# Optimization experiments

Measured on AMD Instinct MI355X. Metric: run time of the kernel, lower is better.

Reference implementation:

```python
import jax, jax.numpy as jnp
import numpy as np

B, T, N, PRED, DM = 16, 512, 128, 256, 32
L = T + PRED  # 768; conv windows 12 then 4: 768 -> 64 -> 16
EPS = 1e-5


def _conv1d(x, w, b, stride):
    # x: [B, C, L'], w: [C, C, k], kernel_size == stride, VALID (matches torch Conv1d)
    out = jax.lax.conv_general_dilated(x, w, (stride,), 'VALID',
                                       dimension_numbers=('NCH', 'OIH', 'NCH'))
    return out + b[None, :, None]


def _conv2d(x, w, b, pad):
    out = jax.lax.conv_general_dilated(x, w, (1, 1), [(pad, pad), (pad, pad)],
                                       dimension_numbers=('NCHW', 'OIHW', 'NCHW'))
    return out + b[None, :, None, None]


def _bn1d(x, g, b):
    # BatchNorm1d, training-mode batch statistics over (batch, length) per channel
    mu = x.mean((0, 2), keepdims=True)
    var = ((x - mu) ** 2).mean((0, 2), keepdims=True)
    return (x - mu) * jax.lax.rsqrt(var + EPS) * g[None, :, None] + b[None, :, None]


def _cubic_spline(y, size):
    # Natural cubic spline through values y: [B, Lk, C] at knots t = linspace(0,1,Lk),
    # evaluated at linspace(0,1,size). Natural BC: second derivative M=0 at endpoints.
    Bb, Lk, C = y.shape
    h = 1.0 / (Lk - 1)
    # tridiagonal system for interior second derivatives (uniform knots):
    # M[i-1] + 4 M[i] + M[i+1] = 6 * (y[i+1] - 2 y[i] + y[i-1]) / h^2
    m = Lk - 2
    rhs = (y[:, 2:, :] - 2.0 * y[:, 1:-1, :] + y[:, :-2, :]) * (6.0 / (h * h))  # [B,m,C]
    A = 4.0 * jnp.eye(m, dtype=y.dtype) + jnp.eye(m, k=1, dtype=y.dtype) + jnp.eye(m, k=-1, dtype=y.dtype)
    Mi = jnp.linalg.solve(A, rhs.transpose(1, 0, 2).reshape(m, Bb * C))  # [m, B*C]
    Mi = Mi.reshape(m, Bb, C).transpose(1, 0, 2)
    M = jnp.pad(Mi, ((0, 0), (1, 1), (0, 0)))  # [B, Lk, C], M[0]=M[-1]=0
    q = jnp.linspace(0.0, 1.0, size).astype(y.dtype)
    idx = jnp.clip(jnp.floor(q * (Lk - 1)).astype(jnp.int32), 0, Lk - 2)  # [size]
    s = (q - idx.astype(y.dtype) * h)[None, :, None]  # offset within interval
    u = h - s
    yi, yi1 = y[:, idx, :], y[:, idx + 1, :]
    M0, M1 = M[:, idx, :], M[:, idx + 1, :]
    hh6 = h * h / 6.0
    return ((M0 * u ** 3 + M1 * s ** 3) / (6.0 * h)
            + (yi - M0 * hh6) * (u / h)
            + (yi1 - M1 * hh6) * (s / h))  # [B, size, C]


def _forward(batch_x, le_w, le_b, c1_w, c1_b, bn1_g, bn1_b, c2_w, c2_b, bn2_g, bn2_b,
             i1_w0, i1_b0, i1_w1, i1_b1, i2_w0, i2_b0, i2_w1, i2_b1, ld_w, ld_b):
    # instance norm over time
    means = batch_x.mean(1, keepdims=True)
    xc = batch_x - means
    stdev = jnp.sqrt(xc.var(axis=1, keepdims=True) + EPS)
    xn = xc / stdev                               # [B, T, N]
    x = xn.transpose(0, 2, 1)                     # [B, N, T]
    x = jnp.einsum('bnt,lt->bnl', x, le_w) + le_b  # length_encoder -> [B, N, L]
    # multi-scale downsampling conv + spline back up to L
    scales = []
    t = x
    for win, cw, cb, g, bb in ((12, c1_w, c1_b, bn1_g, bn1_b), (4, c2_w, c2_b, bn2_g, bn2_b)):
        t = jax.nn.elu(_bn1d(_conv1d(t, cw, cb, win), g, bb))      # [B, N, L//...]
        scales.append(_cubic_spline(t.transpose(0, 2, 1), L).transpose(0, 2, 1))  # [B, N, L]
    a = jnp.stack([x] + scales, axis=1).transpose(0, 1, 3, 2)  # [B, 3, L, N]
    # Inception block 1 (num_kernels=2: 1x1 and 3x3, averaged), Dropout(eval)=id, GELU(exact)
    h1 = 0.5 * (_conv2d(a, i1_w0, i1_b0, 0) + _conv2d(a, i1_w1, i1_b1, 1))  # [B, DM, L, N]
    h1 = jax.nn.gelu(h1, approximate=False)
    # Inception block 2 -> 1 channel
    h2 = 0.5 * (_conv2d(h1, i2_w0, i2_b0, 0) + _conv2d(h1, i2_w1, i2_b1, 1))  # [B, 1, L, N]
    co = x + h2[:, 0].transpose(0, 2, 1)          # residual, [B, N, L]
    f = jnp.einsum('bnl,pl->bnp', co, ld_w) + ld_b  # length_decoder -> [B, N, PRED]
    f = f.transpose(0, 2, 1)                      # [B, PRED, N]
    return f * stdev[:, 0, :][:, None, :] + means[:, 0, :][:, None, :]


def setup_inputs():
    key = jax.random.key(0)
    ks = jax.random.split(key, 20)
    def w(i, shape, scale=0.02):
        return scale * jax.random.normal(ks[i], shape, jnp.float32)
    return dict(
        batch_x=jax.random.normal(ks[0], (B, T, N), jnp.float32),
        batch_x_mark=jax.random.normal(ks[1], (B, T, 4), jnp.float32),
        dec_inp=jax.random.normal(ks[2], (B, PRED, N), jnp.float32),
        batch_y_mark=jax.random.normal(ks[3], (B, PRED, 4), jnp.float32),
        le_w=w(4, (L, T)), le_b=w(5, (L,)),
        c1_w=w(6, (N, N, 12)), c1_b=w(7, (N,)),
        bn1_g=jnp.ones((N,), jnp.float32), bn1_b=jnp.zeros((N,), jnp.float32),
        c2_w=w(8, (N, N, 4)), c2_b=w(9, (N,)),
        bn2_g=jnp.ones((N,), jnp.float32), bn2_b=jnp.zeros((N,), jnp.float32),
        i1_w0=w(10, (DM, 3, 1, 1), 0.1), i1_b0=jnp.zeros((DM,), jnp.float32),
        i1_w1=w(11, (DM, 3, 3, 3), 0.1), i1_b1=jnp.zeros((DM,), jnp.float32),
        i2_w0=w(12, (1, DM, 1, 1), 0.1), i2_b0=jnp.zeros((1,), jnp.float32),
        i2_w1=w(13, (1, DM, 3, 3), 0.1), i2_b1=jnp.zeros((1,), jnp.float32),
        ld_w=w(14, (PRED, L)), ld_b=w(15, (PRED,)),
    )


def reference(batch_x, batch_x_mark, dec_inp, batch_y_mark, le_w, le_b,
              c1_w, c1_b, bn1_g, bn1_b, c2_w, c2_b, bn2_g, bn2_b,
              i1_w0, i1_b0, i1_w1, i1_b1, i2_w0, i2_b0, i2_w1, i2_b1, ld_w, ld_b):
    # batch_x_mark / dec_inp / batch_y_mark are accepted but unused (as in the torch forward)
    return _forward(batch_x, le_w, le_b, c1_w, c1_b, bn1_g, bn1_b, c2_w, c2_b, bn2_g, bn2_b,
                    i1_w0, i1_b0, i1_w1, i1_b1, i2_w0, i2_b0, i2_w1, i2_b1, ld_w, ld_b)
```

## Files before the change

kernel.cpp:

```cpp
#include <hip/hip_runtime.h>
#include <hip/hip_bf16.h>
#include <math.h>

#define BB 16
#define TT 512
#define NN 128
#define PREDN 256
#define DMC 32
#define LL 768
constexpr float EPSF = 1e-5f;
using bf16 = __hip_bfloat16;
using frag_ab = __attribute__((ext_vector_type(8))) short;
using frag_cd = __attribute__((ext_vector_type(4))) float;

__device__ __forceinline__ unsigned pbf2(float a, float b){
  union { bf16 h; unsigned short u; } x, y;
  x.h = __float2bfloat16(a); y.h = __float2bfloat16(b);
  return (unsigned)x.u | ((unsigned)y.u << 16);
}

__device__ __forceinline__ unsigned short bf16b(float v){
  union { bf16 h; unsigned short u; } x;
  x.h = __float2bfloat16(v);
  return x.u;
}

__device__ __forceinline__ float gelu_fast(float s){
  float s2v = s*s;
  float e = exp2f(s*fmaf(s2v, 0.10294396f, 2.30211806f));
  return s*e*__builtin_amdgcn_rcpf(e + 1.f);
}

__global__ void k_pre(const float* __restrict__ bx, const float* __restrict__ v0,
                      const float* __restrict__ v1, const float* __restrict__ w1c,
                      const float* __restrict__ w2c, float* __restrict__ sp,
                      float* __restrict__ s2p, float* __restrict__ vwsT,
                      float* __restrict__ wT1, float* __restrict__ wT2){
  int blk = blockIdx.x;
  if(blk < 64){
    int b = blk >> 2, tq = blk & 3, n = threadIdx.x;
    const float* p = bx + (size_t)b*TT*NN + (size_t)tq*128*NN + n;
    float s = 0.f, s2 = 0.f;
    for(int t=0;t<128;t++){ float v = p[(size_t)t*NN]; s += v; s2 += v*v; }
    sp[tq*2048 + b*NN + n] = s;
    s2p[tq*2048 + b*NN + n] = s2;
  } else if(blk == 64){
    for(int i=threadIdx.x; i<9*DMC; i+=blockDim.x){
      int tap = i/DMC, c = i%DMC;
      float wv = 0.5f*v1[c*9 + tap];
      if(tap == 4) wv += 0.5f*v0[c];
      vwsT[i] = wv;
    }
  } else if(blk <= 192){
    int o = blk - 65;
    for(int k=threadIdx.x; k<1536; k+=blockDim.x)
      wT1[(size_t)k*NN + o] = w1c[(size_t)o*1536 + k];
  } else {
    int o = blk - 193;
    for(int k=threadIdx.x; k<512; k+=blockDim.x)
      wT2[(size_t)k*NN + o] = w2c[(size_t)o*512 + k];
  }
}

__global__ __launch_bounds__(256) void k_gemm1(const float* __restrict__ bx, const float* __restrict__ lew,
    const float* __restrict__ leb, const float* __restrict__ sp, const float* __restrict__ s2p,
    float* __restrict__ x, float* __restrict__ a0){
  __shared__ unsigned Asu[64*20];
  __shared__ unsigned Bsu[64*20];
  int tid = threadIdx.x;
  int row0 = blockIdx.x*64, l0 = blockIdx.y*64;
  int b = row0 >> 7, n0 = row0 & 127;
  int lane = tid & 63, wv = tid >> 6;
  frag_cd acc[4] = {};
  int an = tid & 63, akq = (tid >> 6)*8;
  float mu_a, rs_a;
  {
    int rowa = row0 + an;
    float ssum = 0.f, s2sum = 0.f;
    #pragma unroll
    for(int tq=0;tq<4;tq++){ ssum += sp[tq*2048 + rowa]; s2sum += s2p[tq*2048 + rowa]; }
    mu_a = ssum*(1.f/512.f);
    rs_a = 1.f/sqrtf(fmaxf(s2sum*(1.f/512.f) - mu_a*mu_a, 0.f) + EPSF);
  }
  int btk = tid & 15, blc = tid >> 4;
  unsigned ra[4], rbq[4];
  #pragma unroll
  for(int u=0;u<4;u++){
    float v0 = (bx[((size_t)b*TT + akq + 2*u)*NN + n0 + an] - mu_a)*rs_a;
    float v1 = (bx[((size_t)b*TT + akq + 2*u + 1)*NN + n0 + an] - mu_a)*rs_a;
    ra[u] = pbf2(v0, v1);
    const float* lp = lew + (size_t)(l0 + blc + 16*u)*TT + 2*btk;
    rbq[u] = pbf2(lp[0], lp[1]);
  }
  int fr = wv*16 + (lane & 15);
  int fq = (lane >> 4)*4;
  for(int k0=0;k0<TT;k0+=32){
    *(uint4*)&Asu[an*20 + (akq>>1)] = make_uint4(ra[0], ra[1], ra[2], ra[3]);
    #pragma unroll
    for(int p=0;p<4;p++) Bsu[(blc + 16*p)*20 + btk] = rbq[p];
    __syncthreads();
    if(k0 + 32 < TT){
      #pragma unroll
      for(int u=0;u<4;u++){
        float v0 = (bx[((size_t)b*TT + k0 + 32 + akq + 2*u)*NN + n0 + an] - mu_a)*rs_a;
        float v1 = (bx[((size_t)b*TT + k0 + 32 + akq + 2*u + 1)*NN + n0 + an] - mu_a)*rs_a;
        ra[u] = pbf2(v0, v1);
        const float* lp = lew + (size_t)(l0 + blc + 16*u)*TT + k0 + 32 + 2*btk;
        rbq[u] = pbf2(lp[0], lp[1]);
      }
    }
    frag_ab af = *(const frag_ab*)&Asu[fr*20 + fq];
    #pragma unroll
    for(int nt=0;nt<4;nt++){
      frag_ab bf = *(const frag_ab*)&Bsu[(nt*16 + (lane & 15))*20 + fq];
      acc[nt] = __builtin_amdgcn_mfma_f32_16x16x32_bf16(af, bf, acc[nt], 0, 0, 0);
    }
    __syncthreads();
  }
  int col = lane & 15, quad = lane >> 4;
  #pragma unroll
  for(int nt=0;nt<4;nt++){
    int l = l0 + nt*16 + col;
    float lb = leb[l];
    #pragma unroll
    for(int r=0;r<4;r++){
      int m = wv*16 + quad*4 + r;
      x[(size_t)(row0 + m)*LL + l] = acc[nt][r] + lb;
    }
    float4 st;
    st.x = acc[nt][0] + lb;
    st.y = acc[nt][1] + lb;
    st.z = acc[nt][2] + lb;
    st.w = acc[nt][3] + lb;
    *(float4*)&a0[((size_t)b*LL + l)*NN + n0 + wv*16 + quad*4] = st;
  }
}

__global__ __launch_bounds__(512) void k_conv1(const float* __restrict__ x, const float* __restrict__ wT,
                                               const float* __restrict__ bias, float* __restrict__ t1){
  __shared__ alignas(16) float xs[NN*48];
  int jt = blockIdx.x, b = blockIdx.y;
  int tid = threadIdx.x;
  int o = tid & 127, jj = tid >> 7;
  for(int i=tid;i<NN*48;i+=512){
    int ci = i/48, kk = i%48;
    xs[i] = x[((size_t)b*NN + ci)*LL + jt*48 + kk];
  }
  __syncthreads();
  float a0 = 0.f, a1 = 0.f, a2 = 0.f, a3 = 0.f;
  for(int ci=0;ci<NN;ci++){
    const float* xc = xs + ci*48 + jj*12;
    const float* wc = wT + (size_t)(ci*12)*NN + o;
    #pragma unroll
    for(int kk=0;kk<12;kk+=4){
      a0 = fmaf(xc[kk+0], wc[(size_t)(kk+0)*NN], a0);
      a1 = fmaf(xc[kk+1], wc[(size_t)(kk+1)*NN], a1);
      a2 = fmaf(xc[kk+2], wc[(size_t)(kk+2)*NN], a2);
      a3 = fmaf(xc[kk+3], wc[(size_t)(kk+3)*NN], a3);
    }
  }
  int j = jt*4 + jj;
  t1[((size_t)b*NN + o)*64 + j] = (a0 + a1) + (a2 + a3) + bias[o];
}

__global__ void k_bnstats(const float* __restrict__ t, const float* __restrict__ g, const float* __restrict__ bb,
                          int Bcnt, int Jcnt, float* __restrict__ scale, float* __restrict__ shift){
  int o = blockIdx.x;
  int tot = Bcnt*Jcnt;
  float s = 0.f, s2 = 0.f;
  for(int i=threadIdx.x; i<tot; i+=blockDim.x){
    int b = i / Jcnt, j = i % Jcnt;
    float v = t[((size_t)b*NN + o)*Jcnt + j];
    s += v; s2 += v*v;
  }
  __shared__ float rs[256], rs2[256];
  rs[threadIdx.x] = s; rs2[threadIdx.x] = s2;
  __syncthreads();
  for(int st=128; st>0; st>>=1){
    if(threadIdx.x < st){ rs[threadIdx.x] += rs[threadIdx.x+st]; rs2[threadIdx.x] += rs2[threadIdx.x+st]; }
    __syncthreads();
  }
  if(threadIdx.x == 0){
    float mu = rs[0]/tot;
    float var = fmaxf(rs2[0]/tot - mu*mu, 0.f);
    float sc = g[o] * rsqrtf(var + EPSF);
    scale[o] = sc; shift[o] = bb[o] - mu*sc;
  }
}

__global__ void k_bnelu_t(const float* __restrict__ t, const float* __restrict__ scale,
                          const float* __restrict__ shift, int Jcnt, float* __restrict__ tt){
  int j = blockIdx.x, b = blockIdx.y, o = threadIdx.x;
  float v = t[((size_t)b*NN + o)*Jcnt + j]*scale[o] + shift[o];
  v = v > 0.f ? v : (expf(v) - 1.f);
  tt[((size_t)b*Jcnt + j)*NN + o] = v;
}

template<int LK>
__global__ void k_spline_solve(const float* __restrict__ y, float* __restrict__ M){
  constexpr int m = LK-2;
  const float Kc = 6.f*(LK-1)*(LK-1);
  __shared__ float cp[m];
  __shared__ float dp[m][NN];
  int b = blockIdx.x, c = threadIdx.x;
  if(c == 0){
    float cv = 0.25f; cp[0] = cv;
    for(int i=1;i<m;i++){ cv = 1.f/(4.f - cv); cp[i] = cv; }
  }
  __syncthreads();
  const float* yb = y + (size_t)b*LK*NN + c;
  float y0 = yb[0], y1 = yb[NN];
  float dprev = 0.f;
  for(int i=0;i<m;i++){
    float y2 = yb[(size_t)(i+2)*NN];
    float r = (y2 - 2.f*y1 + y0)*Kc;
    float d = (i == 0) ? r*0.25f : (r - dprev)*cp[i];
    dp[i][c] = d; dprev = d;
    y0 = y1; y1 = y2;
  }
  float* Mb = M + (size_t)b*LK*NN + c;
  float xv = dp[m-1][c];
  Mb[(size_t)m*NN] = xv;
  for(int i=m-2;i>=0;i--){
    xv = dp[i][c] - cp[i]*xv;
    Mb[(size_t)(i+1)*NN] = xv;
  }
  Mb[0] = 0.f;
  Mb[(size_t)(LK-1)*NN] = 0.f;
}

__device__ __forceinline__ float spline_pt(const float* __restrict__ y, const float* __restrict__ M,
                                           int LK, int l, int b, int c){
  float hh = 1.f/(LK-1);
  float q = (float)l * (1.f/(LL-1));
  int idx = (int)floorf(q*(LK-1));
  if(idx > LK-2) idx = LK-2;
  float s = q - idx*hh;
  float u = hh - s;
  const float* yb = y + ((size_t)b*LK + idx)*NN + c;
  const float* Mb = M + ((size_t)b*LK + idx)*NN + c;
  float yi = yb[0], yi1 = yb[NN], M0 = Mb[0], M1 = Mb[NN];
  float hh6 = hh*hh/6.f;
  return (M0*u*u*u + M1*s*s*s)*(1.f/(6.f*hh))
       + (yi  - M0*hh6)*(u*(1.f/hh))
       + (yi1 - M1*hh6)*(s*(1.f/hh));
}

__global__ __launch_bounds__(512) void k_conv2(const float* __restrict__ tt, const float* __restrict__ wT,
                                               const float* __restrict__ bias, float* __restrict__ t2){
  __shared__ alignas(16) float ts[16*NN];
  int jt = blockIdx.x, b = blockIdx.y;
  int tid = threadIdx.x;
  int o = tid & 127, jj = tid >> 7;
  for(int i=tid;i<16*NN;i+=512)
    ts[i] = tt[((size_t)b*64 + jt*16)*NN + i];
  __syncthreads();
  float a0 = 0.f, a1 = 0.f, a2 = 0.f, a3 = 0.f;
  for(int ci=0;ci<NN;ci++){
    const float* wc = wT + (size_t)(ci*4)*NN + o;
    const float* tc2 = ts + (jj*4)*NN + ci;
    a0 = fmaf(tc2[0*NN], wc[0*NN], a0);
    a1 = fmaf(tc2[1*NN], wc[1*NN], a1);
    a2 = fmaf(tc2[2*NN], wc[2*NN], a2);
    a3 = fmaf(tc2[3*NN], wc[3*NN], a3);
  }
  int j = jt*4 + jj;
  t2[((size_t)b*NN + o)*16 + j] = (a0 + a1) + (a2 + a3) + bias[o];
}

constexpr int KOFF[27] = {
    0,   1,   2,  36,  37,  38,  72,  73,  74,
  432, 433, 434, 468, 469, 470, 504, 505, 506,
  864, 865, 866, 900, 901, 902, 936, 937, 938
};

__global__ __launch_bounds__(256) void k_h12(const float* __restrict__ a0,
    const float* __restrict__ y64, const float* __restrict__ M64,
    const float* __restrict__ y16, const float* __restrict__ M16,
    const float* __restrict__ w0, const float* __restrict__ b0,
    const float* __restrict__ w1, const float* __restrict__ b1,
    const float* __restrict__ vwsT, const float* __restrict__ vb0,
    const float* __restrict__ vb1, float* __restrict__ co){
  constexpr int AR = 12, AC = 36;
  __shared__ alignas(16) float as[3][AR][AC];
  __shared__ alignas(16) unsigned Au[352*20];
  int tid = threadIdx.x;
  int l0 = blockIdx.x*8, n0 = blockIdx.y*32, b = blockIdx.z;
  int lane = tid & 63, wv = tid >> 6;

  float* asf = &as[0][0][0];
  for(int i=tid; i<3*AR*AC; i+=256){
    int ch = i/(AR*AC), rem = i%(AR*AC), yy = rem/AC, xx = rem%AC;
    int gl = l0 + yy - 2, gn = n0 + xx - 2;
    float v = 0.f;
    if(gl >= 0 && gl < LL && gn >= 0 && gn < NN){
      if(ch == 0)      v = a0[((size_t)b*LL + gl)*NN + gn];
      else if(ch == 1) v = spline_pt(y64, M64, 64, gl, b, gn);
      else             v = spline_pt(y16, M16, 16, gl, b, gn);
    }
    asf[i] = v;
  }

  int colB = lane & 15, kq = (lane >> 4)*8;
  union { uint4 q; frag_ab f; } bw0, bw1;
  {
    float w8[2][8];
    #pragma unroll
    for(int nt=0;nt<2;nt++){
      #pragma unroll
      for(int j=0;j<8;j++){
        int k = kq + j;
        float w = 0.f;
        if(k < 27){
          int ci = k/9, r9 = k - ci*9, dy = r9/3, dx = r9 - dy*3;
          int c = nt*16 + colB;
          w = 0.5f*w1[((c*3+ci)*3+dy)*3+dx];
          if(dy==1 && dx==1) w += 0.5f*w0[c*3+ci];
        }
        w8[nt][j] = w;
      }
    }
    bw0.q = make_uint4(pbf2(w8[0][0],w8[0][1]), pbf2(w8[0][2],w8[0][3]),
                       pbf2(w8[0][4],w8[0][5]), pbf2(w8[0][6],w8[0][7]));
    bw1.q = make_uint4(pbf2(w8[1][0],w8[1][1]), pbf2(w8[1][2],w8[1][3]),
                       pbf2(w8[1][4],w8[1][5]), pbf2(w8[1][6],w8[1][7]));
  }
  float br0 = 0.5f*(b0[colB] + b1[colB]);
  float br1 = 0.5f*(b0[16 + colB] + b1[16 + colB]);
  __syncthreads();

  for(int base=0; base<352; base+=128){
    int px = base + (tid >> 1);
    int half = tid & 1;
    if(px < 352){
      uint4 oA, oB;
      if(px < 340){
        int yy = px/34, xx = px - yy*34;
        const float* bp = asf + yy*AC + xx;
        if(half == 0){
          oA.x = pbf2(bp[KOFF[0]],  bp[KOFF[1]]);
          oA.y = pbf2(bp[KOFF[2]],  bp[KOFF[3]]);
          oA.z = pbf2(bp[KOFF[4]],  bp[KOFF[5]]);
          oA.w = pbf2(bp[KOFF[6]],  bp[KOFF[7]]);
          oB.x = pbf2(bp[KOFF[8]],  bp[KOFF[9]]);
          oB.y = pbf2(bp[KOFF[10]], bp[KOFF[11]]);
          oB.z = pbf2(bp[KOFF[12]], bp[KOFF[13]]);
          oB.w = pbf2(bp[KOFF[14]], bp[KOFF[15]]);
        } else {
          oA.x = pbf2(bp[KOFF[16]], bp[KOFF[17]]);
          oA.y = pbf2(bp[KOFF[18]], bp[KOFF[19]]);
          oA.z = pbf2(bp[KOFF[20]], bp[KOFF[21]]);
          oA.w = pbf2(bp[KOFF[22]], bp[KOFF[23]]);
          oB.x = pbf2(bp[KOFF[24]], bp[KOFF[25]]);
          oB.y = pbf2(bp[KOFF[26]], 0.f);
          oB.z = 0u; oB.w = 0u;
        }
      } else {
        oA = make_uint4(0u,0u,0u,0u);
        oB = make_uint4(0u,0u,0u,0u);
      }
      *(uint4*)&Au[px*20 + half*8]     = oA;
      *(uint4*)&Au[px*20 + half*8 + 4] = oB;
    }
  }
  __syncthreads();

  unsigned short* h1h = (unsigned short*)Au;
  frag_cd zac = {0.f, 0.f, 0.f, 0.f};
  for(int t = wv; t < 22; t += 4){
    int arow = t*16 + colB;
    union { uint4 q; frag_ab f; } av;
    av.q = *(const uint4*)&Au[arow*20 + (lane>>4)*4];
    frag_cd d0 = __builtin_amdgcn_mfma_f32_16x16x32_bf16(av.f, bw0.f, zac, 0, 0, 0);
    frag_cd d1 = __builtin_amdgcn_mfma_f32_16x16x32_bf16(av.f, bw1.f, zac, 0, 0, 0);
    int px0 = t*16 + (lane>>4)*4;
    #pragma unroll
    for(int r=0;r<4;r++){
      int px = px0 + r;
      h1h[px*40 + colB]      = bf16b(gelu_fast(d0[r] + br0));
      h1h[px*40 + 16 + colB] = bf16b(gelu_fast(d1[r] + br1));
    }
  }
  __syncthreads();

  if(n0 == 0){
    for(int i=tid;i<10*32;i+=256){ int yy=i>>5, ch=i&31; h1h[(yy*34)*40 + ch] = 0; }
  }
  if(n0 == 96){
    for(int i=tid;i<10*32;i+=256){ int yy=i>>5, ch=i&31; h1h[(yy*34+33)*40 + ch] = 0; }
  }
  if(l0 == 0){
    for(int i=tid;i<34*32;i+=256){ int xx=i>>5, ch=i&31; h1h[xx*40 + ch] = 0; }
  }
  if(l0 == 760){
    for(int i=tid;i<34*32;i+=256){ int xx=i>>5, ch=i&31; h1h[(9*34+xx)*40 + ch] = 0; }
  }

  union { uint4 q; frag_ab f; } aw[9];
  {
    bool wlane = (lane & 15) == 0;
    int c8 = (lane >> 4)*8;
    #pragma unroll
    for(int tap=0; tap<9; tap++){
      const float* wp = vwsT + tap*DMC + c8;
      float4 wa = *(const float4*)wp;
      float4 wb = *(const float4*)(wp+4);
      if(!wlane){ wa = make_float4(0.f,0.f,0.f,0.f); wb = make_float4(0.f,0.f,0.f,0.f); }
      aw[tap].q = make_uint4(pbf2(wa.x,wa.y), pbf2(wa.z,wa.w), pbf2(wb.x,wb.y), pbf2(wb.z,wb.w));
    }
  }
  float vbsum = vb0[0] + vb1[0];
  __syncthreads();

  frag_cd cacc[4] = {};
  int kq4 = (lane >> 4)*4;
  int baseoff[4];
  #pragma unroll
  for(int tt=0; tt<4; tt++){
    int px = (wv*4 + tt)*16 + (lane & 15);
    int yy = px >> 5, xx = px & 31;
    baseoff[tt] = (yy*34 + xx)*20 + kq4;
  }
  #pragma unroll
  for(int dy=0; dy<3; dy++)
    #pragma unroll
    for(int dx=0; dx<3; dx++){
      int tap = dy*3 + dx;
      int off = (dy*34 + dx)*20;
      #pragma unroll
      for(int tt=0; tt<4; tt++){
        union { uint4 q; frag_ab f; } bv;
        bv.q = *(const uint4*)&Au[baseoff[tt] + off];
        cacc[tt] = __builtin_amdgcn_mfma_f32_16x16x32_bf16(aw[tap].f, bv.f, cacc[tt], 0, 0, 0);
      }
    }
  if(lane < 16){
    #pragma unroll
    for(int tt=0; tt<4; tt++){
      int px = (wv*4 + tt)*16 + lane;
      int yy = px >> 5, xx = px & 31;
      float res = as[0][yy+2][xx+2];
      size_t idx = ((size_t)b*LL + l0 + yy)*NN + n0 + xx;
      co[idx] = cacc[tt][0] + vbsum + res;
    }
  }
}

__global__ __launch_bounds__(256) void k_gemm2(const float* __restrict__ a0, const float* __restrict__ ldw,
    const float* __restrict__ ldb, const float* __restrict__ sp, const float* __restrict__ s2p,
    float* __restrict__ out){
  __shared__ unsigned Asu[64*20];
  __shared__ unsigned Bsu[64*20];
  int tid = threadIdx.x;
  int row0 = blockIdx.x*64, p0 = blockIdx.y*64;
  int b = row0 >> 7, n0 = row0 & 127;
  int lane = tid & 63, wv = tid >> 6;
  frag_cd acc[4] = {};
  int an = tid & 63, akq = (tid >> 6)*8;
  int btk = tid & 15, blc = tid >> 4;
  unsigned ra[4], rbq[4];
  #pragma unroll
  for(int u=0;u<4;u++){
    float v0 = a0[((size_t)b*LL + akq + 2*u)*NN + n0 + an];
    float v1 = a0[((size_t)b*LL + akq + 2*u + 1)*NN + n0 + an];
    ra[u] = pbf2(v0, v1);
    const float* lp = ldw + (size_t)(p0 + blc + 16*u)*LL + 2*btk;
    rbq[u] = pbf2(lp[0], lp[1]);
  }
  int fr = wv*16 + (lane & 15);
  int fq = (lane >> 4)*4;
  for(int k0=0;k0<LL;k0+=32){
    *(uint4*)&Asu[an*20 + (akq>>1)] = make_uint4(ra[0], ra[1], ra[2], ra[3]);
    #pragma unroll
    for(int p=0;p<4;p++) Bsu[(blc + 16*p)*20 + btk] = rbq[p];
    __syncthreads();
    if(k0 + 32 < LL){
      #pragma unroll
      for(int u=0;u<4;u++){
        float v0 = a0[((size_t)b*LL + k0 + 32 + akq + 2*u)*NN + n0 + an];
        float v1 = a0[((size_t)b*LL + k0 + 32 + akq + 2*u + 1)*NN + n0 + an];
        ra[u] = pbf2(v0, v1);
        const float* lp = ldw + (size_t)(p0 + blc + 16*u)*LL + k0 + 32 + 2*btk;
        rbq[u] = pbf2(lp[0], lp[1]);
      }
    }
    frag_ab af = *(const frag_ab*)&Asu[fr*20 + fq];
    #pragma unroll
    for(int nt=0;nt<4;nt++){
      frag_ab bf = *(const frag_ab*)&Bsu[(nt*16 + (lane & 15))*20 + fq];
      acc[nt] = __builtin_amdgcn_mfma_f32_16x16x32_bf16(af, bf, acc[nt], 0, 0, 0);
    }
    __syncthreads();
  }
  int col = lane & 15, quad = lane >> 4;
  float mu_r[4], sd_r[4];
  #pragma unroll
  for(int r=0;r<4;r++){
    int row = row0 + wv*16 + quad*4 + r;
    float ssum = 0.f, s2sum = 0.f;
    #pragma unroll
    for(int tq=0;tq<4;tq++){ ssum += sp[tq*2048 + row]; s2sum += s2p[tq*2048 + row]; }
    float mu = ssum*(1.f/512.f);
    float var = fmaxf(s2sum*(1.f/512.f) - mu*mu, 0.f);
    mu_r[r] = mu; sd_r[r] = sqrtf(var + EPSF);
  }
  #pragma unroll
  for(int nt=0;nt<4;nt++){
    int p = p0 + nt*16 + col;
    float lb = ldb[p];
    float4 st;
    st.x = (acc[nt][0] + lb)*sd_r[0] + mu_r[0];
    st.y = (acc[nt][1] + lb)*sd_r[1] + mu_r[1];
    st.z = (acc[nt][2] + lb)*sd_r[2] + mu_r[2];
    st.w = (acc[nt][3] + lb)*sd_r[3] + mu_r[3];
    *(float4*)&out[((size_t)b*PREDN + p)*NN + n0 + wv*16 + quad*4] = st;
  }
}

extern "C" void kernel_launch(void* const* d_in, const int* in_sizes, int n_in,
                              void* d_out, int out_size, void* d_ws, size_t ws_size,
                              hipStream_t stream){
  (void)in_sizes; (void)n_in; (void)out_size; (void)ws_size;
  const float* batch_x = (const float*)d_in[0];
  const float* le_w  = (const float*)d_in[4];
  const float* le_b  = (const float*)d_in[5];
  const float* c1_w  = (const float*)d_in[6];
  const float* c1_b  = (const float*)d_in[7];
  const float* bn1_g = (const float*)d_in[8];
  const float* bn1_b = (const float*)d_in[9];
  const float* c2_w  = (const float*)d_in[10];
  const float* c2_b  = (const float*)d_in[11];
  const float* bn2_g = (const float*)d_in[12];
  const float* bn2_b = (const float*)d_in[13];
  const float* i1_w0 = (const float*)d_in[14];
  const float* i1_b0 = (const float*)d_in[15];
  const float* i1_w1 = (const float*)d_in[16];
  const float* i1_b1 = (const float*)d_in[17];
  const float* i2_w0 = (const float*)d_in[18];
  const float* i2_b0 = (const float*)d_in[19];
  const float* i2_w1 = (const float*)d_in[20];
  const float* i2_b1 = (const float*)d_in[21];
  const float* ld_w  = (const float*)d_in[22];
  const float* ld_b  = (const float*)d_in[23];
  float* out = (float*)d_out;

  float* ws   = (float*)d_ws;
  float* sp   = ws;
  float* s2p  = sp + 8192;
  float* vwsT = s2p + 8192;
  float* wT1  = vwsT + 320;
  float* wT2  = wT1 + 196608;
  float* x    = wT2 + 65536;
  float* a0   = x + (size_t)BB*NN*LL;
  float* t1   = a0 + (size_t)BB*LL*NN;
  float* t1t  = t1 + (size_t)BB*NN*64;
  float* sc1  = t1t + (size_t)BB*64*NN;
  float* sh1  = sc1 + NN;
  float* Msp1 = sh1 + NN;
  float* t2   = Msp1 + (size_t)BB*64*NN;
  float* t2t  = t2 + (size_t)BB*NN*16;
  float* sc2  = t2t + (size_t)BB*16*NN;
  float* sh2  = sc2 + NN;
  float* Msp2 = sh2 + NN;
  float* co   = Msp2 + (size_t)BB*16*NN;

  k_pre<<<321, 128, 0, stream>>>(batch_x, i2_w0, i2_w1, c1_w, c2_w, sp, s2p, vwsT, wT1, wT2);
  k_gemm1<<<dim3(32,12), 256, 0, stream>>>(batch_x, le_w, le_b, sp, s2p, x, a0);
  k_conv1<<<dim3(16,BB), 512, 0, stream>>>(x, wT1, c1_b, t1);
  k_bnstats<<<NN, 256, 0, stream>>>(t1, bn1_g, bn1_b, BB, 64, sc1, sh1);
  k_bnelu_t<<<dim3(64,BB), NN, 0, stream>>>(t1, sc1, sh1, 64, t1t);
  k_spline_solve<64><<<BB, NN, 0, stream>>>(t1t, Msp1);
  k_conv2<<<dim3(4,BB), 512, 0, stream>>>(t1t, wT2, c2_b, t2);
  k_bnstats<<<NN, 256, 0, stream>>>(t2, bn2_g, bn2_b, BB, 16, sc2, sh2);
  k_bnelu_t<<<dim3(16,BB), NN, 0, stream>>>(t2, sc2, sh2, 16, t2t);
  k_spline_solve<16><<<BB, NN, 0, stream>>>(t2t, Msp2);
  k_h12<<<dim3(96,4,BB), 256, 0, stream>>>(a0, t1t, Msp1, t2t, Msp2,
                                           i1_w0, i1_b0, i1_w1, i1_b1,
                                           vwsT, i2_b0, i2_b1, co);
  k_gemm2<<<dim3(32,4), 256, 0, stream>>>(co, ld_w, ld_b, sp, s2p, out);
}
```

Baseline: 310.7 us.

## Split h12 LDS buffer into per-quad planes and halve gemm2 output tile

Reorganizes the k_h12 shared-memory activation buffer from a padded interleaved row layout (20 words per pixel) into four separate 8-channel planes, so each MFMA fragment load reads contiguous 16-byte chunks per quad. This is meant to reduce LDS bank conflicts and shrink LDS footprint; it also adds a launch_bounds occupancy hint of 5 blocks. Separately, k_gemm2 now uses 32-column output tiles with twice as many blocks, trading more A-tile reloads for more parallelism across CUs.

```diff
diff --git a/kernel.cpp b/kernel.cpp
--- a/kernel.cpp
+++ b/kernel.cpp
@@ -274,7 +274,8 @@
   864, 865, 866, 900, 901, 902, 936, 937, 938
 };
 
-__global__ __launch_bounds__(256) void k_h12(const float* __restrict__ a0,
+#define PBQ 1416
+__global__ __launch_bounds__(256, 5) void k_h12(const float* __restrict__ a0,
     const float* __restrict__ y64, const float* __restrict__ M64,
     const float* __restrict__ y16, const float* __restrict__ M16,
     const float* __restrict__ w0, const float* __restrict__ b0,
@@ -283,7 +284,7 @@
     const float* __restrict__ vb1, float* __restrict__ co){
   constexpr int AR = 12, AC = 36;
   __shared__ alignas(16) float as[3][AR][AC];
-  __shared__ alignas(16) unsigned Au[352*20];
+  __shared__ alignas(16) unsigned Au[4*PBQ];
   int tid = threadIdx.x;
   int l0 = blockIdx.x*8, n0 = blockIdx.y*32, b = blockIdx.z;
   int lane = tid & 63, wv = tid >> 6;
@@ -359,47 +360,53 @@
         oA = make_uint4(0u,0u,0u,0u);
         oB = make_uint4(0u,0u,0u,0u);
       }
-      *(uint4*)&Au[px*20 + half*8]     = oA;
-      *(uint4*)&Au[px*20 + half*8 + 4] = oB;
+      *(uint4*)&Au[(2*half)*PBQ + px*4]     = oA;
+      *(uint4*)&Au[(2*half+1)*PBQ + px*4]   = oB;
     }
   }
   __syncthreads();
 
   unsigned short* h1h = (unsigned short*)Au;
   frag_cd zac = {0.f, 0.f, 0.f, 0.f};
+  int qg = lane >> 4;
+  int g0 = colB >> 3, s0 = colB & 7;
   for(int t = wv; t < 22; t += 4){
     int arow = t*16 + colB;
     union { uint4 q; frag_ab f; } av;
-    av.q = *(const uint4*)&Au[arow*20 + (lane>>4)*4];
+    av.q = *(const uint4*)&Au[qg*PBQ + arow*4];
     frag_cd d0 = __builtin_amdgcn_mfma_f32_16x16x32_bf16(av.f, bw0.f, zac, 0, 0, 0);
     frag_cd d1 = __builtin_amdgcn_mfma_f32_16x16x32_bf16(av.f, bw1.f, zac, 0, 0, 0);
-    int px0 = t*16 + (lane>>4)*4;
+    int px0 = t*16 + qg*4;
     #pragma unroll
     for(int r=0;r<4;r++){
       int px = px0 + r;
-      h1h[px*40 + colB]      = bf16b(gelu_fast(d0[r] + br0));
-      h1h[px*40 + 16 + colB] = bf16b(gelu_fast(d1[r] + br1));
+      h1h[(g0*PBQ + px*4)*2 + s0]     = bf16b(gelu_fast(d0[r] + br0));
+      h1h[((g0+2)*PBQ + px*4)*2 + s0] = bf16b(gelu_fast(d1[r] + br1));
     }
   }
   __syncthreads();
 
   if(n0 == 0){
-    for(int i=tid;i<10*32;i+=256){ int yy=i>>5, ch=i&31; h1h[(yy*34)*40 + ch] = 0; }
+    for(int i=tid;i<10*32;i+=256){ int yy=i>>5, ch=i&31;
+      h1h[((ch>>3)*PBQ + (yy*34)*4)*2 + (ch&7)] = 0; }
   }
   if(n0 == 96){
-    for(int i=tid;i<10*32;i+=256){ int yy=i>>5, ch=i&31; h1h[(yy*34+33)*40 + ch] = 0; }
+    for(int i=tid;i<10*32;i+=256){ int yy=i>>5, ch=i&31;
+      h1h[((ch>>3)*PBQ + (yy*34+33)*4)*2 + (ch&7)] = 0; }
   }
   if(l0 == 0){
-    for(int i=tid;i<34*32;i+=256){ int xx=i>>5, ch=i&31; h1h[xx*40 + ch] = 0; }
+    for(int i=tid;i<34*32;i+=256){ int xx=i>>5, ch=i&31;
+      h1h[((ch>>3)*PBQ + xx*4)*2 + (ch&7)] = 0; }
   }
   if(l0 == 760){
-    for(int i=tid;i<34*32;i+=256){ int xx=i>>5, ch=i&31; h1h[(9*34+xx)*40 + ch] = 0; }
+    for(int i=tid;i<34*32;i+=256){ int xx=i>>5, ch=i&31;
+      h1h[((ch>>3)*PBQ + (9*34+xx)*4)*2 + (ch&7)] = 0; }
   }
 
   union { uint4 q; frag_ab f; } aw[9];
   {
     bool wlane = (lane & 15) == 0;
-    int c8 = (lane >> 4)*8;
+    int c8 = qg*8;
     #pragma unroll
     for(int tap=0; tap<9; tap++){
       const float* wp = vwsT + tap*DMC + c8;
@@ -413,20 +420,19 @@
   __syncthreads();
 
   frag_cd cacc[4] = {};
-  int kq4 = (lane >> 4)*4;
   int baseoff[4];
   #pragma unroll
   for(int tt=0; tt<4; tt++){
     int px = (wv*4 + tt)*16 + (lane & 15);
     int yy = px >> 5, xx = px & 31;
-    baseoff[tt] = (yy*34 + xx)*20 + kq4;
+    baseoff[tt] = qg*PBQ + (yy*34 + xx)*4;
   }
   #pragma unroll
   for(int dy=0; dy<3; dy++)
     #pragma unroll
     for(int dx=0; dx<3; dx++){
       int tap = dy*3 + dx;
-      int off = (dy*34 + dx)*20;
+      int off = (dy*34 + dx)*4;
       #pragma unroll
       for(int tt=0; tt<4; tt++){
         union { uint4 q; frag_ab f; } bv;
@@ -450,20 +456,23 @@
     const float* __restrict__ ldb, const float* __restrict__ sp, const float* __restrict__ s2p,
     float* __restrict__ out){
   __shared__ unsigned Asu[64*20];
-  __shared__ unsigned Bsu[64*20];
+  __shared__ unsigned Bsu[32*20];
   int tid = threadIdx.x;
-  int row0 = blockIdx.x*64, p0 = blockIdx.y*64;
+  int row0 = blockIdx.x*64, p0 = blockIdx.y*32;
   int b = row0 >> 7, n0 = row0 & 127;
   int lane = tid & 63, wv = tid >> 6;
-  frag_cd acc[4] = {};
+  frag_cd acc[2] = {};
   int an = tid & 63, akq = (tid >> 6)*8;
   int btk = tid & 15, blc = tid >> 4;
-  unsigned ra[4], rbq[4];
+  unsigned ra[4], rbq[2];
   #pragma unroll
   for(int u=0;u<4;u++){
     float v0 = a0[((size_t)b*LL + akq + 2*u)*NN + n0 + an];
     float v1 = a0[((size_t)b*LL + akq + 2*u + 1)*NN + n0 + an];
     ra[u] = pbf2(v0, v1);
+  }
+  #pragma unroll
+  for(int u=0;u<2;u++){
     const float* lp = ldw + (size_t)(p0 + blc + 16*u)*LL + 2*btk;
     rbq[u] = pbf2(lp[0], lp[1]);
   }
@@ -472,7 +481,7 @@
   for(int k0=0;k0<LL;k0+=32){
     *(uint4*)&Asu[an*20 + (akq>>1)] = make_uint4(ra[0], ra[1], ra[2], ra[3]);
     #pragma unroll
-    for(int p=0;p<4;p++) Bsu[(blc + 16*p)*20 + btk] = rbq[p];
+    for(int p=0;p<2;p++) Bsu[(blc + 16*p)*20 + btk] = rbq[p];
     __syncthreads();
     if(k0 + 32 < LL){
       #pragma unroll
@@ -480,13 +489,16 @@
         float v0 = a0[((size_t)b*LL + k0 + 32 + akq + 2*u)*NN + n0 + an];
         float v1 = a0[((size_t)b*LL + k0 + 32 + akq + 2*u + 1)*NN + n0 + an];
         ra[u] = pbf2(v0, v1);
+      }
+      #pragma unroll
+      for(int u=0;u<2;u++){
         const float* lp = ldw + (size_t)(p0 + blc + 16*u)*LL + k0 + 32 + 2*btk;
         rbq[u] = pbf2(lp[0], lp[1]);
       }
     }
     frag_ab af = *(const frag_ab*)&Asu[fr*20 + fq];
     #pragma unroll
-    for(int nt=0;nt<4;nt++){
+    for(int nt=0;nt<2;nt++){
       frag_ab bf = *(const frag_ab*)&Bsu[(nt*16 + (lane & 15))*20 + fq];
       acc[nt] = __builtin_amdgcn_mfma_f32_16x16x32_bf16(af, bf, acc[nt], 0, 0, 0);
     }
@@ -505,7 +517,7 @@
     mu_r[r] = mu; sd_r[r] = sqrtf(var + EPSF);
   }
   #pragma unroll
-  for(int nt=0;nt<4;nt++){
+  for(int nt=0;nt<2;nt++){
     int p = p0 + nt*16 + col;
     float lb = ldb[p];
     float4 st;
@@ -577,5 +589,5 @@
   k_h12<<<dim3(96,4,BB), 256, 0, stream>>>(a0, t1t, Msp1, t2t, Msp2,
                                            i1_w0, i1_b0, i1_w1, i1_b1,
                                            vwsT, i2_b0, i2_b1, co);
-  k_gemm2<<<dim3(32,4), 256, 0, stream>>>(co, ld_w, ld_b, sp, s2p, out);
-}
+  k_gemm2<<<dim3(32,8), 256, 0, stream>>>(co, ld_w, ld_b, sp, s2p, out);
+}
```

After: 299.6 us. 3.6% less time.
